# Performance work log

Measured on AMD Instinct MI355X. Metric: run time of the kernel, lower is better.

## Reference

```python
import jax, jax.numpy as jnp
import numpy as np

N, E = 50000, 800000
DIN_N, DIN_E = 64, 64
DO_N, DO_E, H = 32, 32, 4
NEG_SLOPE = 0.01


def setup_inputs() -> dict:
    key = jax.random.key(0)
    ks = jax.random.split(key, 12)
    s = 0.05
    return {
        "nfeats": jax.random.normal(ks[0], (N, DIN_N), jnp.float32),
        "efeats": jax.random.normal(ks[1], (E, DIN_E), jnp.float32),
        "src": jax.random.randint(ks[2], (E,), 0, N, jnp.int32),
        "dst": jax.random.randint(ks[3], (E,), 0, N, jnp.int32),
        "Wn": jax.random.normal(ks[4], (DIN_N, DO_N * H), jnp.float32) * s,
        "bn": jnp.zeros((DO_N * H,), jnp.float32),
        "We": jax.random.normal(ks[5], (DIN_E + 2 * DIN_N, DO_E * H), jnp.float32) * s,
        "Wa": jax.random.normal(ks[6], (DO_E, H), jnp.float32) * s,
        "Won": jax.random.normal(ks[7], (DO_N * H, DO_N), jnp.float32) * s,
        "bon": jnp.zeros((DO_N,), jnp.float32),
        "Woe": jax.random.normal(ks[8], (DO_E * H, DO_E), jnp.float32) * s,
        "boe": jnp.zeros((DO_E,), jnp.float32),
    }


def _egat(nfeats, efeats, src, dst, Wn, bn, We, Wa, Won, bon, Woe, boe):
    # edge attention: concat [h_src, f, h_dst] -> linear(no bias) -> leaky_relu
    stack = jnp.concatenate([nfeats[src], efeats, nfeats[dst]], axis=-1)  # [E, 2Dn+De]
    f = jax.nn.leaky_relu(stack @ We, NEG_SLOPE).reshape(E, H, DO_E)      # [E, H, Fo]
    # fc_attn: [E,H,Fo] @ [Fo,H] -> [E,H,H], summed over last axis -> [E,H]
    a = jnp.einsum("ehf,fk->eh", f, Wa * 1.0) * 0 + (f @ Wa).sum(-1)
    a = (f @ Wa).sum(-1)  # [E, H]
    # projected node features for messages
    nproj = (nfeats @ Wn + bn).reshape(N, H, DO_N)  # [N, H, Do]
    # segment softmax of a over destination nodes
    m = jax.ops.segment_max(a, dst, num_segments=N)  # [N, H]
    m = jnp.where(jnp.isfinite(m), m, 0.0)
    ex = jnp.exp(a - m[dst])                         # [E, H]
    den = jax.ops.segment_sum(ex, dst, num_segments=N)  # [N, H]
    alpha = ex / den[dst]                            # safe: dst has >=1 edge here
    # weighted scatter-sum of src messages
    msg = alpha[:, :, None] * nproj[src]             # [E, H, Do]
    agg = jax.ops.segment_sum(msg, dst, num_segments=N)  # [N, H, Do]
    # zero in-degree nodes keep projected features (DGL update_all semantics)
    deg = jax.ops.segment_sum(jnp.ones((E,), nfeats.dtype), dst, num_segments=N)
    h = jnp.where(deg[:, None, None] > 0, agg, nproj)
    h_out = h.reshape(N, H * DO_N) @ Won + bon
    e_out = f.reshape(E, H * DO_E) @ Woe + boe
    return h_out, e_out


def reference(nfeats, efeats, src, dst, Wn, bn, We, Wa, Won, bon, Woe, boe):
    return _egat(nfeats, efeats, src, dst, Wn, bn, We, Wa, Won, bon, Woe, boe)
```

## Files before the change

### kernel.cpp

```cpp
#include <hip/hip_runtime.h>
#include <hip/hip_bf16.h>


#define NN 50000
#define NE 800000
#define NB ((NN + 255) / 256)

typedef __attribute__((ext_vector_type(8))) __bf16 bf16x8;
typedef __attribute__((ext_vector_type(4))) float f32x4;

__device__ __forceinline__ float lrelu(float x) { return x > 0.f ? x : 0.01f * x; }
__device__ __forceinline__ unsigned short f2bf(float x) {
    __bf16 b = (__bf16)x; return *reinterpret_cast<unsigned short*>(&b);
}
__device__ __forceinline__ float bf2f(unsigned short u) {
    __bf16 b = *reinterpret_cast<__bf16*>(&u); return (float)b;
}

__global__ __launch_bounds__(256) void k_count(const int* __restrict__ dst,
                                               int* __restrict__ deg)
{
    int i = blockIdx.x * blockDim.x + threadIdx.x;
    int stride = gridDim.x * blockDim.x;
    for (; i < NE; i += stride) atomicAdd(&deg[dst[i]], 1);
}

__global__ __launch_bounds__(256) void k_scan_blk(const int* __restrict__ deg,
                                                  int* __restrict__ rowptr,
                                                  int* __restrict__ bsum)
{
    __shared__ int wsum[4];
    const int tid = threadIdx.x, lane = tid & 63, wid = tid >> 6;
    const int i = blockIdx.x * 256 + tid;
    int v = (i < NN) ? deg[i] : 0;
    int x = v;
    #pragma unroll
    for (int off = 1; off < 64; off <<= 1) {
        int t = __shfl_up(x, off);
        if (lane >= off) x += t;
    }
    if (lane == 63) wsum[wid] = x;
    __syncthreads();
    if (tid == 0) {
        int s = 0;
        #pragma unroll
        for (int w = 0; w < 4; ++w) { int t = wsum[w]; wsum[w] = s; s += t; }
        bsum[blockIdx.x] = s;
    }
    __syncthreads();
    if (i < NN) rowptr[i] = wsum[wid] + x - v;
}

__global__ __launch_bounds__(256) void k_scan_top(int* __restrict__ bsum,
                                                  int* __restrict__ rowptr)
{
    __shared__ int wsum[4];
    const int tid = threadIdx.x, lane = tid & 63, wid = tid >> 6;
    int v = (tid < NB) ? bsum[tid] : 0;
    int x = v;
    #pragma unroll
    for (int off = 1; off < 64; off <<= 1) {
        int t = __shfl_up(x, off);
        if (lane >= off) x += t;
    }
    if (lane == 63) wsum[wid] = x;
    __syncthreads();
    if (tid == 0) {
        int s = 0;
        #pragma unroll
        for (int w = 0; w < 4; ++w) { int t = wsum[w]; wsum[w] = s; s += t; }
    }
    __syncthreads();
    int excl = wsum[wid] + x - v;
    if (tid < NB) bsum[tid] = excl;
    if (tid == NB - 1) rowptr[NN] = excl + v;
}

__global__ __launch_bounds__(256) void k_scan_add(int* __restrict__ rowptr,
                                                  const int* __restrict__ bsum,
                                                  int* __restrict__ cursor)
{
    const int i = blockIdx.x * 256 + threadIdx.x;
    if (i < NN) {
        int r = rowptr[i] + bsum[blockIdx.x];
        rowptr[i] = r;
        cursor[i] = r;
    }
}

__global__ __launch_bounds__(256) void k_prepw(const float* __restrict__ We,
                                               const float* __restrict__ Wa,
                                               const float* __restrict__ Woe,
                                               unsigned short* __restrict__ Wefrag,
                                               unsigned short* __restrict__ Woefrag,
                                               float* __restrict__ wa_sum)
{
    const int tid = threadIdx.x;
    if (tid < 32) {
        float4 w = *reinterpret_cast<const float4*>(&Wa[tid * 4]);
        wa_sum[tid] = w.x + w.y + w.z + w.w;
    }
    for (int idx = tid; idx < 8192; idx += 256) {
        int j = idx & 7, l = (idx >> 3) & 63, th = idx >> 9;
        int h = th & 1, t = th >> 1;
        int k = 32 * h + (l >> 4) * 8 + j;
        int c = 16 * t + (l & 15);
        Wefrag[idx] = f2bf(We[(64 + k) * 128 + c]);
    }
    for (int idx = tid; idx < 4096; idx += 256) {
        int j = idx & 7, l = (idx >> 3) & 63, uk = idx >> 9;
        int ks = uk & 3, u = uk >> 2;
        int k = 32 * ks + (l >> 4) * 8 + j;
        int c = 16 * u + (l & 15);
        Woefrag[idx] = f2bf(Woe[k * 32 + c]);
    }
}

__global__ __launch_bounds__(256) void k_proj(
    const float* __restrict__ nf, const float* __restrict__ Wn,
    const float* __restrict__ bn, const float* __restrict__ We,
    float* __restrict__ nproj, unsigned short* __restrict__ Psb,
    unsigned short* __restrict__ Pdb)
{
    __shared__ __align__(16) float sA[64 * 68];
    __shared__ __align__(16) float sW[64 * 128];
    const int tid = threadIdx.x;
    const int mode = blockIdx.y;
    const int nBase = blockIdx.x * 64;

    const float* W = (mode == 0) ? Wn : (mode == 1 ? We : We + 128 * 128);

    #pragma unroll
    for (int q = 0; q < 4; ++q) {
        int idx = q * 256 + tid;
        int e = idx >> 4, c4 = idx & 15;
        int row = nBase + e;
        float4 v = make_float4(0.f, 0.f, 0.f, 0.f);
        if (row < NN) v = *reinterpret_cast<const float4*>(&nf[row * 64 + c4 * 4]);
        *reinterpret_cast<float4*>(&sA[e * 68 + c4 * 4]) = v;
    }
    #pragma unroll
    for (int q = 0; q < 8; ++q) {
        int idx = q * 256 + tid;
        *reinterpret_cast<float4*>(&sW[idx * 4]) =
            *reinterpret_cast<const float4*>(&W[idx * 4]);
    }
    __syncthreads();

    const int jt = tid & 15, et = tid >> 4;
    float acc[4][8];
    #pragma unroll
    for (int i = 0; i < 4; ++i)
        #pragma unroll
        for (int j = 0; j < 8; ++j) acc[i][j] = 0.f;

    #pragma unroll 2
    for (int kk4 = 0; kk4 < 16; ++kk4) {
        float4 a4[4];
        #pragma unroll
        for (int i = 0; i < 4; ++i)
            a4[i] = *reinterpret_cast<const float4*>(&sA[(4 * et + i) * 68 + 4 * kk4]);
        #pragma unroll
        for (int c = 0; c < 4; ++c) {
            int kk = 4 * kk4 + c;
            float4 b0 = *reinterpret_cast<const float4*>(&sW[kk * 128 + 4 * jt]);
            float4 b1 = *reinterpret_cast<const float4*>(&sW[kk * 128 + 64 + 4 * jt]);
            #pragma unroll
            for (int i = 0; i < 4; ++i) {
                float av = (&a4[i].x)[c];
                acc[i][0] = fmaf(av, b0.x, acc[i][0]);
                acc[i][1] = fmaf(av, b0.y, acc[i][1]);
                acc[i][2] = fmaf(av, b0.z, acc[i][2]);
                acc[i][3] = fmaf(av, b0.w, acc[i][3]);
                acc[i][4] = fmaf(av, b1.x, acc[i][4]);
                acc[i][5] = fmaf(av, b1.y, acc[i][5]);
                acc[i][6] = fmaf(av, b1.z, acc[i][6]);
                acc[i][7] = fmaf(av, b1.w, acc[i][7]);
            }
        }
    }

    if (mode == 0) {
        float4 bias0 = *reinterpret_cast<const float4*>(&bn[4 * jt]);
        float4 bias1 = *reinterpret_cast<const float4*>(&bn[64 + 4 * jt]);
        #pragma unroll
        for (int i = 0; i < 4; ++i) {
            int row = nBase + 4 * et + i;
            if (row >= NN) continue;
            float4 r0 = make_float4(acc[i][0] + bias0.x, acc[i][1] + bias0.y,
                                    acc[i][2] + bias0.z, acc[i][3] + bias0.w);
            float4 r1 = make_float4(acc[i][4] + bias1.x, acc[i][5] + bias1.y,
                                    acc[i][6] + bias1.z, acc[i][7] + bias1.w);
            *reinterpret_cast<float4*>(&nproj[(size_t)row * 128 + 4 * jt]) = r0;
            *reinterpret_cast<float4*>(&nproj[(size_t)row * 128 + 64 + 4 * jt]) = r1;
        }
    } else {
        unsigned short* outp = (mode == 1) ? Psb : Pdb;
        #pragma unroll
        for (int i = 0; i < 4; ++i) {
            int row = nBase + 4 * et + i;
            if (row >= NN) continue;
            ushort4 u0, u1;
            u0.x = f2bf(acc[i][0]); u0.y = f2bf(acc[i][1]);
            u0.z = f2bf(acc[i][2]); u0.w = f2bf(acc[i][3]);
            u1.x = f2bf(acc[i][4]); u1.y = f2bf(acc[i][5]);
            u1.z = f2bf(acc[i][6]); u1.w = f2bf(acc[i][7]);
            *reinterpret_cast<ushort4*>(&outp[(size_t)row * 128 + 4 * jt]) = u0;
            *reinterpret_cast<ushort4*>(&outp[(size_t)row * 128 + 64 + 4 * jt]) = u1;
        }
    }
}

__global__ __launch_bounds__(256) void k_edge(
    const float* __restrict__ ef, const int* __restrict__ src,
    const int* __restrict__ dst,
    const unsigned short* __restrict__ Wefrag,
    const unsigned short* __restrict__ Woefrag,
    const float* __restrict__ wa_sum,
    const float* __restrict__ boe,
    const unsigned short* __restrict__ Psb, const unsigned short* __restrict__ Pdb,
    int* __restrict__ cursor, int* __restrict__ srcs,
    float* __restrict__ exs, float* __restrict__ e_out)
{
    __shared__ __align__(16) unsigned short fbuf[64 * 136];
    __shared__ __align__(16) int sidx[128];
    __shared__ __align__(16) float swa[32];

    const int tid = threadIdx.x;
    const int w = tid >> 6, l = tid & 63;
    const int g = l >> 4, c16 = l & 15;
    const int eBase = blockIdx.x * 64;
    const int rowBase = eBase + 16 * w;

    if (tid < 64) { sidx[tid] = src[eBase + tid]; sidx[64 + tid] = dst[eBase + tid]; }
    else if (tid < 96) swa[tid - 64] = wa_sum[tid - 64];

    bf16x8 afrag[2];
    #pragma unroll
    for (int h = 0; h < 2; ++h) {
        const float* ap = &ef[(size_t)(rowBase + c16) * 64 + 32 * h + 8 * g];
        float4 a0 = *reinterpret_cast<const float4*>(ap);
        float4 a1 = *reinterpret_cast<const float4*>(ap + 4);
        bf16x8 v;
        v[0] = (__bf16)a0.x; v[1] = (__bf16)a0.y;
        v[2] = (__bf16)a0.z; v[3] = (__bf16)a0.w;
        v[4] = (__bf16)a1.x; v[5] = (__bf16)a1.y;
        v[6] = (__bf16)a1.z; v[7] = (__bf16)a1.w;
        afrag[h] = v;
    }

    f32x4 acc[8];
    #pragma unroll
    for (int t = 0; t < 8; ++t) {
        f32x4 z = {0.f, 0.f, 0.f, 0.f};
        acc[t] = z;
        #pragma unroll
        for (int h = 0; h < 2; ++h) {
            bf16x8 b = *reinterpret_cast<const bf16x8*>(
                &Wefrag[((size_t)(t * 2 + h) * 64 + l) * 8]);
            acc[t] = __builtin_amdgcn_mfma_f32_16x16x32_bf16(afrag[h], b, acc[t], 0, 0, 0);
        }
    }

    #pragma unroll
    for (int t = 0; t < 8; ++t)
        #pragma unroll
        for (int r = 0; r < 4; ++r)
            fbuf[(16 * w + 4 * g + r) * 136 + 16 * t + c16] = f2bf(acc[t][r]);

    __syncthreads();

    {
        const int e = tid >> 2, q = tid & 3;
        const int s = sidx[e], d = sidx[64 + e];
        float4 wlo = *reinterpret_cast<const float4*>(&swa[4 * q]);
        float4 whi = *reinterpret_cast<const float4*>(&swa[16 + 4 * q]);
        float ah[4] = {0.f, 0.f, 0.f, 0.f};
        #pragma unroll
        for (int j = 0; j < 8; ++j) {
            int col = 16 * j + 4 * q;
            ushort4 psu = *reinterpret_cast<const ushort4*>(&Psb[(size_t)s * 128 + col]);
            ushort4 pdu = *reinterpret_cast<const ushort4*>(&Pdb[(size_t)d * 128 + col]);
            ushort4 rw = *reinterpret_cast<const ushort4*>(&fbuf[e * 136 + col]);
            float f0 = lrelu(bf2f(rw.x) + bf2f(psu.x) + bf2f(pdu.x));
            float f1 = lrelu(bf2f(rw.y) + bf2f(psu.y) + bf2f(pdu.y));
            float f2 = lrelu(bf2f(rw.z) + bf2f(psu.z) + bf2f(pdu.z));
            float f3 = lrelu(bf2f(rw.w) + bf2f(psu.w) + bf2f(pdu.w));
            const float4& wv = (j & 1) ? whi : wlo;
            int h = j >> 1;
            ah[h] = fmaf(f0, wv.x, ah[h]);
            ah[h] = fmaf(f1, wv.y, ah[h]);
            ah[h] = fmaf(f2, wv.z, ah[h]);
            ah[h] = fmaf(f3, wv.w, ah[h]);
            ushort4 fw;
            fw.x = f2bf(f0); fw.y = f2bf(f1); fw.z = f2bf(f2); fw.w = f2bf(f3);
            *reinterpret_cast<ushort4*>(&fbuf[e * 136 + col]) = fw;
        }
        #pragma unroll
        for (int h = 0; h < 4; ++h) {
            float v = ah[h];
            v += __shfl_xor(v, 1);
            v += __shfl_xor(v, 2);
            ah[h] = v;
        }
        int pos = 0;
        if (q == 0) pos = atomicAdd(&cursor[d], 1);
        pos = __shfl(pos, l & ~3);
        if (q == 0) srcs[pos] = s;
        float myA = (q == 0) ? ah[0] : (q == 1) ? ah[1] : (q == 2) ? ah[2] : ah[3];
        exs[(size_t)pos * 4 + q] = expf(myA);
    }

    __syncthreads();

    {
        bf16x8 af[4];
        #pragma unroll
        for (int ks = 0; ks < 4; ++ks)
            af[ks] = *reinterpret_cast<const bf16x8*>(
                &fbuf[(16 * w + c16) * 136 + 32 * ks + 8 * g]);
        #pragma unroll
        for (int u = 0; u < 2; ++u) {
            f32x4 o = {0.f, 0.f, 0.f, 0.f};
            #pragma unroll
            for (int ks = 0; ks < 4; ++ks) {
                bf16x8 b = *reinterpret_cast<const bf16x8*>(
                    &Woefrag[((size_t)(u * 4 + ks) * 64 + l) * 8]);
                o = __builtin_amdgcn_mfma_f32_16x16x32_bf16(af[ks], b, o, 0, 0, 0);
            }
            float bo = boe[16 * u + c16];
            #pragma unroll
            for (int r = 0; r < 4; ++r)
                e_out[(size_t)(eBase + 16 * w + 4 * g + r) * 32 + 16 * u + c16] =
                    o[r] + bo;
        }
    }
}

__global__ __launch_bounds__(256) void k_agg(
    const int* __restrict__ rowptr, const int* __restrict__ srcs,
    const float* __restrict__ exs, const float* __restrict__ nproj,
    float* __restrict__ hbuf)
{
    const int tid = threadIdx.x;
    const int j = tid & 127;
    const int n = blockIdx.x * 2 + (tid >> 7);
    if (n >= NN) return;
    const int beg = rowptr[n], end = rowptr[n + 1];
    const int h = j >> 5;
    float val = 0.f, den = 0.f;
    int p = beg;
    for (; p + 4 <= end; p += 4) {
        int s0 = srcs[p],     s1 = srcs[p + 1];
        int s2 = srcs[p + 2], s3 = srcs[p + 3];
        float e0 = exs[(size_t)p * 4 + h];
        float e1 = exs[(size_t)(p + 1) * 4 + h];
        float e2 = exs[(size_t)(p + 2) * 4 + h];
        float e3 = exs[(size_t)(p + 3) * 4 + h];
        float n0 = nproj[(size_t)s0 * 128 + j];
        float n1 = nproj[(size_t)s1 * 128 + j];
        float n2 = nproj[(size_t)s2 * 128 + j];
        float n3 = nproj[(size_t)s3 * 128 + j];
        val = fmaf(e0, n0, val); val = fmaf(e1, n1, val);
        val = fmaf(e2, n2, val); val = fmaf(e3, n3, val);
        den += e0 + e1 + e2 + e3;
    }
    for (; p < end; ++p) {
        int s = srcs[p];
        float ex = exs[(size_t)p * 4 + h];
        val = fmaf(ex, nproj[(size_t)s * 128 + j], val);
        den += ex;
    }
    float out = (end > beg) ? (val / den) : nproj[(size_t)n * 128 + j];
    hbuf[(size_t)n * 128 + j] = out;
}

__global__ __launch_bounds__(256) void k_node_out(
    const float* __restrict__ hbuf, const float* __restrict__ Won,
    const float* __restrict__ bon, float* __restrict__ h_out)
{
    __shared__ __align__(16) float sh[64 * 132];
    __shared__ __align__(16) float sWon[128 * 32];
    __shared__ __align__(16) float sbon[32];
    const int tid = threadIdx.x;
    const int nBase = blockIdx.x * 64;

    #pragma unroll
    for (int q = 0; q < 8; ++q) {
        int idx = q * 256 + tid;
        int n = idx >> 5, c4 = idx & 31;
        int row = nBase + n;
        float4 v = make_float4(0.f, 0.f, 0.f, 0.f);
        if (row < NN)
            v = *reinterpret_cast<const float4*>(&hbuf[(size_t)row * 128 + c4 * 4]);
        *reinterpret_cast<float4*>(&sh[n * 132 + c4 * 4]) = v;
    }
    #pragma unroll
    for (int q = 0; q < 4; ++q) {
        int idx = q * 256 + tid;
        *reinterpret_cast<float4*>(&sWon[idx * 4]) =
            *reinterpret_cast<const float4*>(&Won[idx * 4]);
    }
    if (tid < 32) sbon[tid] = bon[tid];
    __syncthreads();

    int n = tid >> 2, q = tid & 3;
    int j0 = q * 8;
    int row = nBase + n;
    float4 r0 = make_float4(0.f, 0.f, 0.f, 0.f), r1 = r0;
    #pragma unroll 4
    for (int k = 0; k < 128; k += 4) {
        float4 fv = *reinterpret_cast<const float4*>(&sh[n * 132 + k]);
        #pragma unroll
        for (int c = 0; c < 4; ++c) {
            float fk = (&fv.x)[c];
            float4 w0 = *reinterpret_cast<const float4*>(&sWon[(k + c) * 32 + j0]);
            float4 w1 = *reinterpret_cast<const float4*>(&sWon[(k + c) * 32 + j0 + 4]);
            r0.x = fmaf(fk, w0.x, r0.x); r0.y = fmaf(fk, w0.y, r0.y);
            r0.z = fmaf(fk, w0.z, r0.z); r0.w = fmaf(fk, w0.w, r0.w);
            r1.x = fmaf(fk, w1.x, r1.x); r1.y = fmaf(fk, w1.y, r1.y);
            r1.z = fmaf(fk, w1.z, r1.z); r1.w = fmaf(fk, w1.w, r1.w);
        }
    }
    if (row < NN) {
        float4 b0 = *reinterpret_cast<const float4*>(&sbon[j0]);
        float4 b1 = *reinterpret_cast<const float4*>(&sbon[j0 + 4]);
        r0.x += b0.x; r0.y += b0.y; r0.z += b0.z; r0.w += b0.w;
        r1.x += b1.x; r1.y += b1.y; r1.z += b1.z; r1.w += b1.w;
        size_t o = (size_t)row * 32 + j0;
        *reinterpret_cast<float4*>(&h_out[o]) = r0;
        *reinterpret_cast<float4*>(&h_out[o + 4]) = r1;
    }
}

extern "C" void kernel_launch(void* const* d_in, const int* in_sizes, int n_in,
                              void* d_out, int out_size, void* d_ws, size_t ws_size,
                              hipStream_t stream) {
    const float* nfeats = (const float*)d_in[0];
    const float* efeats = (const float*)d_in[1];
    const int*   src    = (const int*)d_in[2];
    const int*   dst    = (const int*)d_in[3];
    const float* Wn     = (const float*)d_in[4];
    const float* bn     = (const float*)d_in[5];
    const float* We     = (const float*)d_in[6];
    const float* Wa     = (const float*)d_in[7];
    const float* Won    = (const float*)d_in[8];
    const float* bon    = (const float*)d_in[9];
    const float* Woe    = (const float*)d_in[10];
    const float* boe    = (const float*)d_in[11];

    float* h_out = (float*)d_out;
    float* e_out = h_out + (size_t)NN * 32;

    float* nproj  = (float*)d_ws;
    unsigned short* Psb = (unsigned short*)(nproj + (size_t)NN * 128);
    unsigned short* Pdb = Psb + (size_t)NN * 128;
    float* exs    = (float*)(Pdb + (size_t)NN * 128);
    int*   deg    = (int*)(exs + (size_t)NE * 4);
    int*   rowptr = deg + NN;
    int*   cursor = rowptr + NN + 1;
    int*   srcs   = cursor + NN;
    int*   bsum   = srcs + NE;
    float* wa_sum = (float*)(bsum + 256);
    unsigned short* Wefrag =
        (unsigned short*)(((uintptr_t)(wa_sum + 32) + 15) & ~(uintptr_t)15);
    unsigned short* Woefrag = Wefrag + 8192;
    float* hbuf   = (float*)Psb;

    hipMemsetAsync(deg, 0, NN * sizeof(int), stream);

    k_count<<<1024, 256, 0, stream>>>(dst, deg);
    k_scan_blk<<<NB, 256, 0, stream>>>(deg, rowptr, bsum);
    k_scan_top<<<1, 256, 0, stream>>>(bsum, rowptr);
    k_scan_add<<<NB, 256, 0, stream>>>(rowptr, bsum, cursor);

    k_prepw<<<1, 256, 0, stream>>>(We, Wa, Woe, Wefrag, Woefrag, wa_sum);

    dim3 gProj((NN + 63) / 64, 3);
    k_proj<<<gProj, 256, 0, stream>>>(nfeats, Wn, bn, We, nproj, Psb, Pdb);

    k_edge<<<NE / 64, 256, 0, stream>>>(efeats, src, dst, Wefrag, Woefrag,
                                        wa_sum, boe, Psb, Pdb,
                                        cursor, srcs, exs, e_out);

    k_agg<<<(NN + 1) / 2, 256, 0, stream>>>(rowptr, srcs, exs, nproj, hbuf);

    k_node_out<<<(NN + 63) / 64, 256, 0, stream>>>(hbuf, Won, bon, h_out);
}
```

Measured before the change: 649.1 us.

## Fold Won into node projection and fuse aggregation with output

Precomputes per-head Wn·Won (and bias) so the node projection directly yields per-head 32-wide outputs stored as bf16. Because the output projection is linear, the per-node aggregation can then gather 128 bf16 values per source, divide each head by its softmax denominator, sum the four heads and add bon. This removes the separate k_node_out kernel and the fp32 hbuf round trip, and halves the gather traffic in aggregation. It trades some precision, since the projected messages are now rounded to bf16.

Result: faster. 634.0 us (-2.3%).

```diff
diff --git a/kernel.cpp b/kernel.cpp
--- a/kernel.cpp
+++ b/kernel.cpp
@@ -91,9 +91,14 @@
 __global__ __launch_bounds__(256) void k_prepw(const float* __restrict__ We,
                                                const float* __restrict__ Wa,
                                                const float* __restrict__ Woe,
+                                               const float* __restrict__ Wn,
+                                               const float* __restrict__ bn,
+                                               const float* __restrict__ Won,
                                                unsigned short* __restrict__ Wefrag,
                                                unsigned short* __restrict__ Woefrag,
-                                               float* __restrict__ wa_sum)
+                                               float* __restrict__ wa_sum,
+                                               float* __restrict__ Wcomb,
+                                               float* __restrict__ bcomb)
 {
     const int tid = threadIdx.x;
     if (tid < 32) {
@@ -114,12 +119,28 @@
         int c = 16 * u + (l & 15);
         Woefrag[idx] = f2bf(Woe[k * 32 + c]);
     }
+    for (int idx = tid; idx < 8192; idx += 256) {
+        int c = idx & 31, h = (idx >> 5) & 3, f = idx >> 7;
+        float s = 0.f;
+        #pragma unroll 8
+        for (int f2 = 0; f2 < 32; ++f2)
+            s = fmaf(Wn[f * 128 + 32 * h + f2], Won[(32 * h + f2) * 32 + c], s);
+        Wcomb[f * 128 + 32 * h + c] = s;
+    }
+    if (tid < 128) {
+        int c = tid & 31, h = tid >> 5;
+        float s = 0.f;
+        #pragma unroll 8
+        for (int f2 = 0; f2 < 32; ++f2)
+            s = fmaf(bn[32 * h + f2], Won[(32 * h + f2) * 32 + c], s);
+        bcomb[tid] = s;
+    }
 }
 
 __global__ __launch_bounds__(256) void k_proj(
-    const float* __restrict__ nf, const float* __restrict__ Wn,
-    const float* __restrict__ bn, const float* __restrict__ We,
-    float* __restrict__ nproj, unsigned short* __restrict__ Psb,
+    const float* __restrict__ nf, const float* __restrict__ Wcomb,
+    const float* __restrict__ bcomb, const float* __restrict__ We,
+    unsigned short* __restrict__ mproj, unsigned short* __restrict__ Psb,
     unsigned short* __restrict__ Pdb)
 {
     __shared__ __align__(16) float sA[64 * 68];
@@ -128,7 +149,8 @@
     const int mode = blockIdx.y;
     const int nBase = blockIdx.x * 64;
 
-    const float* W = (mode == 0) ? Wn : (mode == 1 ? We : We + 128 * 128);
+    const float* W = (mode == 0) ? Wcomb : (mode == 1 ? We : We + 128 * 128);
+    unsigned short* outp = (mode == 0) ? mproj : (mode == 1 ? Psb : Pdb);
 
     #pragma unroll
     for (int q = 0; q < 4; ++q) {
@@ -180,34 +202,22 @@
         }
     }
 
+    float4 bias0 = make_float4(0.f, 0.f, 0.f, 0.f), bias1 = bias0;
     if (mode == 0) {
-        float4 bias0 = *reinterpret_cast<const float4*>(&bn[4 * jt]);
-        float4 bias1 = *reinterpret_cast<const float4*>(&bn[64 + 4 * jt]);
-        #pragma unroll
-        for (int i = 0; i < 4; ++i) {
-            int row = nBase + 4 * et + i;
-            if (row >= NN) continue;
-            float4 r0 = make_float4(acc[i][0] + bias0.x, acc[i][1] + bias0.y,
-                                    acc[i][2] + bias0.z, acc[i][3] + bias0.w);
-            float4 r1 = make_float4(acc[i][4] + bias1.x, acc[i][5] + bias1.y,
-                                    acc[i][6] + bias1.z, acc[i][7] + bias1.w);
-            *reinterpret_cast<float4*>(&nproj[(size_t)row * 128 + 4 * jt]) = r0;
-            *reinterpret_cast<float4*>(&nproj[(size_t)row * 128 + 64 + 4 * jt]) = r1;
-        }
-    } else {
-        unsigned short* outp = (mode == 1) ? Psb : Pdb;
-        #pragma unroll
-        for (int i = 0; i < 4; ++i) {
-            int row = nBase + 4 * et + i;
-            if (row >= NN) continue;
-            ushort4 u0, u1;
-            u0.x = f2bf(acc[i][0]); u0.y = f2bf(acc[i][1]);
-            u0.z = f2bf(acc[i][2]); u0.w = f2bf(acc[i][3]);
-            u1.x = f2bf(acc[i][4]); u1.y = f2bf(acc[i][5]);
-            u1.z = f2bf(acc[i][6]); u1.w = f2bf(acc[i][7]);
-            *reinterpret_cast<ushort4*>(&outp[(size_t)row * 128 + 4 * jt]) = u0;
-            *reinterpret_cast<ushort4*>(&outp[(size_t)row * 128 + 64 + 4 * jt]) = u1;
-        }
+        bias0 = *reinterpret_cast<const float4*>(&bcomb[4 * jt]);
+        bias1 = *reinterpret_cast<const float4*>(&bcomb[64 + 4 * jt]);
+    }
+    #pragma unroll
+    for (int i = 0; i < 4; ++i) {
+        int row = nBase + 4 * et + i;
+        if (row >= NN) continue;
+        ushort4 u0, u1;
+        u0.x = f2bf(acc[i][0] + bias0.x); u0.y = f2bf(acc[i][1] + bias0.y);
+        u0.z = f2bf(acc[i][2] + bias0.z); u0.w = f2bf(acc[i][3] + bias0.w);
+        u1.x = f2bf(acc[i][4] + bias1.x); u1.y = f2bf(acc[i][5] + bias1.y);
+        u1.z = f2bf(acc[i][6] + bias1.z); u1.w = f2bf(acc[i][7] + bias1.w);
+        *reinterpret_cast<ushort4*>(&outp[(size_t)row * 128 + 4 * jt]) = u0;
+        *reinterpret_cast<ushort4*>(&outp[(size_t)row * 128 + 64 + 4 * jt]) = u1;
     }
 }
 
@@ -337,100 +347,59 @@
     }
 }
 
-__global__ __launch_bounds__(256) void k_agg(
+__global__ __launch_bounds__(256) void k_aggout(
     const int* __restrict__ rowptr, const int* __restrict__ srcs,
-    const float* __restrict__ exs, const float* __restrict__ nproj,
-    float* __restrict__ hbuf)
+    const float* __restrict__ exs, const unsigned short* __restrict__ mproj,
+    const float* __restrict__ bon, float* __restrict__ h_out)
 {
     const int tid = threadIdx.x;
-    const int j = tid & 127;
-    const int n = blockIdx.x * 2 + (tid >> 7);
+    const int c = tid & 31;
+    const int n = blockIdx.x * 8 + (tid >> 5);
     if (n >= NN) return;
     const int beg = rowptr[n], end = rowptr[n + 1];
-    const int h = j >> 5;
-    float val = 0.f, den = 0.f;
+    float a0 = 0.f, a1 = 0.f, a2 = 0.f, a3 = 0.f;
+    float d0 = 0.f, d1 = 0.f, d2 = 0.f, d3 = 0.f;
     int p = beg;
     for (; p + 4 <= end; p += 4) {
         int s0 = srcs[p],     s1 = srcs[p + 1];
         int s2 = srcs[p + 2], s3 = srcs[p + 3];
-        float e0 = exs[(size_t)p * 4 + h];
-        float e1 = exs[(size_t)(p + 1) * 4 + h];
-        float e2 = exs[(size_t)(p + 2) * 4 + h];
-        float e3 = exs[(size_t)(p + 3) * 4 + h];
-        float n0 = nproj[(size_t)s0 * 128 + j];
-        float n1 = nproj[(size_t)s1 * 128 + j];
-        float n2 = nproj[(size_t)s2 * 128 + j];
-        float n3 = nproj[(size_t)s3 * 128 + j];
-        val = fmaf(e0, n0, val); val = fmaf(e1, n1, val);
-        val = fmaf(e2, n2, val); val = fmaf(e3, n3, val);
-        den += e0 + e1 + e2 + e3;
+        float4 e0 = *reinterpret_cast<const float4*>(&exs[(size_t)p * 4]);
+        float4 e1 = *reinterpret_cast<const float4*>(&exs[(size_t)(p + 1) * 4]);
+        float4 e2 = *reinterpret_cast<const float4*>(&exs[(size_t)(p + 2) * 4]);
+        float4 e3 = *reinterpret_cast<const float4*>(&exs[(size_t)(p + 3) * 4]);
+        const unsigned short* m0 = &mproj[(size_t)s0 * 128 + c];
+        const unsigned short* m1 = &mproj[(size_t)s1 * 128 + c];
+        const unsigned short* m2 = &mproj[(size_t)s2 * 128 + c];
+        const unsigned short* m3 = &mproj[(size_t)s3 * 128 + c];
+        a0 = fmaf(e0.x, bf2f(m0[0]),  a0); a1 = fmaf(e0.y, bf2f(m0[32]), a1);
+        a2 = fmaf(e0.z, bf2f(m0[64]), a2); a3 = fmaf(e0.w, bf2f(m0[96]), a3);
+        a0 = fmaf(e1.x, bf2f(m1[0]),  a0); a1 = fmaf(e1.y, bf2f(m1[32]), a1);
+        a2 = fmaf(e1.z, bf2f(m1[64]), a2); a3 = fmaf(e1.w, bf2f(m1[96]), a3);
+        a0 = fmaf(e2.x, bf2f(m2[0]),  a0); a1 = fmaf(e2.y, bf2f(m2[32]), a1);
+        a2 = fmaf(e2.z, bf2f(m2[64]), a2); a3 = fmaf(e2.w, bf2f(m2[96]), a3);
+        a0 = fmaf(e3.x, bf2f(m3[0]),  a0); a1 = fmaf(e3.y, bf2f(m3[32]), a1);
+        a2 = fmaf(e3.z, bf2f(m3[64]), a2); a3 = fmaf(e3.w, bf2f(m3[96]), a3);
+        d0 += e0.x + e1.x + e2.x + e3.x;
+        d1 += e0.y + e1.y + e2.y + e3.y;
+        d2 += e0.z + e1.z + e2.z + e3.z;
+        d3 += e0.w + e1.w + e2.w + e3.w;
     }
     for (; p < end; ++p) {
         int s = srcs[p];
-        float ex = exs[(size_t)p * 4 + h];
-        val = fmaf(ex, nproj[(size_t)s * 128 + j], val);
-        den += ex;
-    }
-    float out = (end > beg) ? (val / den) : nproj[(size_t)n * 128 + j];
-    hbuf[(size_t)n * 128 + j] = out;
-}
-
-__global__ __launch_bounds__(256) void k_node_out(
-    const float* __restrict__ hbuf, const float* __restrict__ Won,
-    const float* __restrict__ bon, float* __restrict__ h_out)
-{
-    __shared__ __align__(16) float sh[64 * 132];
-    __shared__ __align__(16) float sWon[128 * 32];
-    __shared__ __align__(16) float sbon[32];
-    const int tid = threadIdx.x;
-    const int nBase = blockIdx.x * 64;
-
-    #pragma unroll
-    for (int q = 0; q < 8; ++q) {
-        int idx = q * 256 + tid;
-        int n = idx >> 5, c4 = idx & 31;
-        int row = nBase + n;
-        float4 v = make_float4(0.f, 0.f, 0.f, 0.f);
-        if (row < NN)
-            v = *reinterpret_cast<const float4*>(&hbuf[(size_t)row * 128 + c4 * 4]);
-        *reinterpret_cast<float4*>(&sh[n * 132 + c4 * 4]) = v;
-    }
-    #pragma unroll
-    for (int q = 0; q < 4; ++q) {
-        int idx = q * 256 + tid;
-        *reinterpret_cast<float4*>(&sWon[idx * 4]) =
-            *reinterpret_cast<const float4*>(&Won[idx * 4]);
-    }
-    if (tid < 32) sbon[tid] = bon[tid];
-    __syncthreads();
-
-    int n = tid >> 2, q = tid & 3;
-    int j0 = q * 8;
-    int row = nBase + n;
-    float4 r0 = make_float4(0.f, 0.f, 0.f, 0.f), r1 = r0;
-    #pragma unroll 4
-    for (int k = 0; k < 128; k += 4) {
-        float4 fv = *reinterpret_cast<const float4*>(&sh[n * 132 + k]);
-        #pragma unroll
-        for (int c = 0; c < 4; ++c) {
-            float fk = (&fv.x)[c];
-            float4 w0 = *reinterpret_cast<const float4*>(&sWon[(k + c) * 32 + j0]);
-            float4 w1 = *reinterpret_cast<const float4*>(&sWon[(k + c) * 32 + j0 + 4]);
-            r0.x = fmaf(fk, w0.x, r0.x); r0.y = fmaf(fk, w0.y, r0.y);
-            r0.z = fmaf(fk, w0.z, r0.z); r0.w = fmaf(fk, w0.w, r0.w);
-            r1.x = fmaf(fk, w1.x, r1.x); r1.y = fmaf(fk, w1.y, r1.y);
-            r1.z = fmaf(fk, w1.z, r1.z); r1.w = fmaf(fk, w1.w, r1.w);
-        }
-    }
-    if (row < NN) {
-        float4 b0 = *reinterpret_cast<const float4*>(&sbon[j0]);
-        float4 b1 = *reinterpret_cast<const float4*>(&sbon[j0 + 4]);
-        r0.x += b0.x; r0.y += b0.y; r0.z += b0.z; r0.w += b0.w;
-        r1.x += b1.x; r1.y += b1.y; r1.z += b1.z; r1.w += b1.w;
-        size_t o = (size_t)row * 32 + j0;
-        *reinterpret_cast<float4*>(&h_out[o]) = r0;
-        *reinterpret_cast<float4*>(&h_out[o + 4]) = r1;
-    }
+        float4 e = *reinterpret_cast<const float4*>(&exs[(size_t)p * 4]);
+        const unsigned short* m = &mproj[(size_t)s * 128 + c];
+        a0 = fmaf(e.x, bf2f(m[0]),  a0); a1 = fmaf(e.y, bf2f(m[32]), a1);
+        a2 = fmaf(e.z, bf2f(m[64]), a2); a3 = fmaf(e.w, bf2f(m[96]), a3);
+        d0 += e.x; d1 += e.y; d2 += e.z; d3 += e.w;
+    }
+    float out;
+    if (end > beg) {
+        out = a0 / d0 + a1 / d1 + a2 / d2 + a3 / d3;
+    } else {
+        const unsigned short* m = &mproj[(size_t)n * 128 + c];
+        out = bf2f(m[0]) + bf2f(m[32]) + bf2f(m[64]) + bf2f(m[96]);
+    }
+    h_out[(size_t)n * 32 + c] = out + bon[c];
 }
 
 extern "C" void kernel_launch(void* const* d_in, const int* in_sizes, int n_in,
@@ -452,8 +421,8 @@
     float* h_out = (float*)d_out;
     float* e_out = h_out + (size_t)NN * 32;
 
-    float* nproj  = (float*)d_ws;
-    unsigned short* Psb = (unsigned short*)(nproj + (size_t)NN * 128);
+    unsigned short* mproj = (unsigned short*)d_ws;
+    unsigned short* Psb = mproj + (size_t)NN * 128;
     unsigned short* Pdb = Psb + (size_t)NN * 128;
     float* exs    = (float*)(Pdb + (size_t)NN * 128);
     int*   deg    = (int*)(exs + (size_t)NE * 4);
@@ -465,7 +434,8 @@
     unsigned short* Wefrag =
         (unsigned short*)(((uintptr_t)(wa_sum + 32) + 15) & ~(uintptr_t)15);
     unsigned short* Woefrag = Wefrag + 8192;
-    float* hbuf   = (float*)Psb;
+    float* Wcomb  = (float*)(Woefrag + 4096);
+    float* bcomb  = Wcomb + 8192;
 
     hipMemsetAsync(deg, 0, NN * sizeof(int), stream);
 
@@ -474,16 +444,16 @@
     k_scan_top<<<1, 256, 0, stream>>>(bsum, rowptr);
     k_scan_add<<<NB, 256, 0, stream>>>(rowptr, bsum, cursor);
 
-    k_prepw<<<1, 256, 0, stream>>>(We, Wa, Woe, Wefrag, Woefrag, wa_sum);
+    k_prepw<<<1, 256, 0, stream>>>(We, Wa, Woe, Wn, bn, Won,
+                                   Wefrag, Woefrag, wa_sum, Wcomb, bcomb);
 
     dim3 gProj((NN + 63) / 64, 3);
-    k_proj<<<gProj, 256, 0, stream>>>(nfeats, Wn, bn, We, nproj, Psb, Pdb);
+    k_proj<<<gProj, 256, 0, stream>>>(nfeats, Wcomb, bcomb, We, mproj, Psb, Pdb);
 
     k_edge<<<NE / 64, 256, 0, stream>>>(efeats, src, dst, Wefrag, Woefrag,
                                         wa_sum, boe, Psb, Pdb,
                                         cursor, srcs, exs, e_out);
 
-    k_agg<<<(NN + 1) / 2, 256, 0, stream>>>(rowptr, srcs, exs, nproj, hbuf);
-
-    k_node_out<<<(NN + 63) / 64, 256, 0, stream>>>(hbuf, Won, bon, h_out);
-}
+    k_aggout<<<(NN + 7) / 8, 256, 0, stream>>>(rowptr, srcs, exs, mproj,
+                                               bon, h_out);
+}
```
